# Kernel tuning notes

Measured on AMD Instinct MI355X. Metric: run time of the kernel, lower is better.

## Reference

```python
import jax, jax.numpy as jnp
import numpy as np

MAX_DISP = 4          # 9x9 displacement window -> 81 output channels
WIN = 2 * MAX_DISP + 1


def setup_inputs() -> dict:
    key = jax.random.key(0)
    k1, k2 = jax.random.split(key)
    B, C, H, W = 4, 256, 192, 192
    tensorFirst = jax.random.normal(k1, (B, C, H, W), dtype=jnp.float32)
    tensorSecond = jax.random.normal(k2, (B, C, H, W), dtype=jnp.float32)
    return {"tensorFirst": tensorFirst, "tensorSecond": tensorSecond}


def reference(tensorFirst, tensorSecond):
    # PWC-Net correlation: out[b, (dy+4)*9+(dx+4), y, x] =
    #   mean_c first[b,c,y,x] * second[b,c,y+dy,x+dx]  (second zero-padded by 4)
    B, C, H, W = tensorFirst.shape
    padded = jnp.pad(tensorSecond, ((0, 0), (0, 0), (MAX_DISP, MAX_DISP), (MAX_DISP, MAX_DISP)))
    outs = []
    for dy in range(WIN):
        for dx in range(WIN):
            shifted = padded[:, :, dy:dy + H, dx:dx + W]  # [B,C,H,W]
            outs.append(jnp.mean(tensorFirst * shifted, axis=1))  # [B,H,W]
    return jnp.stack(outs, axis=1)  # [B,81,H,W]
```

## Files before the change

### kernel.cpp

```cpp
#include <hip/hip_runtime.h>


#define MAXD 4
#define WINW 9
#define NDISP 81

constexpr int B_ = 4, C_ = 256, H_ = 192, W_ = 192;
constexpr int PHW = H_ * W_;
constexpr int YS = 3;
constexpr int DS = 3;
constexpr int XS = 64;
constexpr int VR = YS + DS - 1;
constexpr int NUT = 5;
constexpr int KB = 32;
constexpr int NK = C_ / KB;
constexpr int NTHREADS = 512;

constexpr int S_USHORT = VR * NUT * 512;
constexpr int F_USHORT = YS * 4 * 512;
constexpr int LDS_USHORT = S_USHORT + F_USHORT;
constexpr int S_TASKS = S_USHORT / 8;
constexpr int F_TASKS = F_USHORT / 8;

constexpr int NYS = H_ / YS;
constexpr int NDS = WINW / DS;
constexpr int NXS = W_ / XS;
constexpr int NBLK = B_ * NYS * NDS * NXS;
constexpr int PER_XCD = NBLK / 8;

typedef __attribute__((ext_vector_type(8))) short bf16x8;
typedef __attribute__((ext_vector_type(4))) float f32x4;

__device__ __forceinline__ unsigned f2bf(float f) {
    unsigned u = __float_as_uint(f);
    return (u + 0x7FFFu + ((u >> 16) & 1u)) >> 16;
}

__global__ __launch_bounds__(NTHREADS, 4)
void corr_kernel(const float* __restrict__ F, const float* __restrict__ S,
                 float* __restrict__ O) {
    __shared__ __align__(16) unsigned short lds[LDS_USHORT];

    const int tid  = threadIdx.x;
    const int lane = tid & 63;
    const int wid  = tid >> 6;
    const int xt   = wid & 3;
    const int uh   = wid >> 2;
    const int utw  = xt + uh;

    const int id = blockIdx.x;
    const int lg = (id & 7) * PER_XCD + (id >> 3);
    const int xs     = lg % NXS;
    const int t1     = lg / NXS;
    const int dstrip = t1 % NDS;
    const int t2     = t1 / NDS;
    const int ystrip = t2 % NYS;
    const int b      = t2 / NYS;
    const int Y0 = ystrip * YS, D0 = dstrip * DS, x0 = xs * XS;
    const int vbase = Y0 + D0 - MAXD;
    const int ubase = x0 - 8;

    const float* Fb = F + (long)b * C_ * PHW;
    const float* Sb = S + (long)b * C_ * PHW;

    const float* sP[4]; int sL[4]; bool sOk[4], sAct[4];
    #pragma unroll
    for (int q = 0; q < 4; ++q) {
        const int t   = tid + q * NTHREADS;
        const bool a  = (t < S_TASKS);
        const int tt  = a ? t : 0;
        const int u16 = tt & 15;
        const int kh  = (tt >> 4) & 3;
        const int rest = tt >> 6;
        const int ut  = rest % 5;
        const int vr  = rest / 5;
        const int v   = vbase + vr;
        const int u   = ubase + ut * 16 + u16;
        const bool inb = a && ((unsigned)v < (unsigned)H_) &&
                              ((unsigned)u < (unsigned)W_);
        sAct[q] = a;
        sOk[q]  = inb;
        sL[q]   = tt * 8;
        sP[q]   = Sb + (long)(kh * 8) * PHW + (long)(inb ? v : 0) * W_
                     + (inb ? u : 0);
    }
    const float* fP[2]; int fL[2]; bool fAct[2];
    #pragma unroll
    for (int q = 0; q < 2; ++q) {
        const int t   = tid + q * NTHREADS;
        const bool a  = (t < F_TASKS);
        const int tt  = a ? t : 0;
        const int x16 = tt & 15;
        const int kh  = (tt >> 4) & 3;
        const int rest = tt >> 6;
        const int xtq = rest & 3;
        const int yy  = rest >> 2;
        fAct[q] = a;
        fL[q]   = S_USHORT + tt * 8;
        fP[q]   = Fb + (long)(kh * 8) * PHW + (long)(Y0 + yy) * W_
                     + (x0 + xtq * 16 + x16);
    }

    f32x4 acc[3][3];
    #pragma unroll
    for (int yy = 0; yy < 3; ++yy)
        #pragma unroll
        for (int dd = 0; dd < 3; ++dd)
            acc[yy][dd] = (f32x4){0.f, 0.f, 0.f, 0.f};

    for (int step = 0; step < NK; ++step) {
        const int c0 = step * KB;
        #pragma unroll
        for (int q = 0; q < 4; ++q) {
            if (!sAct[q]) continue;
            unsigned w0 = 0, w1 = 0, w2 = 0, w3 = 0;
            if (sOk[q]) {
                const float* p = sP[q] + (long)c0 * PHW;
                float f[8];
                #pragma unroll
                for (int j = 0; j < 8; ++j) f[j] = p[j * PHW];
                w0 = f2bf(f[0]) | (f2bf(f[1]) << 16);
                w1 = f2bf(f[2]) | (f2bf(f[3]) << 16);
                w2 = f2bf(f[4]) | (f2bf(f[5]) << 16);
                w3 = f2bf(f[6]) | (f2bf(f[7]) << 16);
            }
            uint4 v; v.x = w0; v.y = w1; v.z = w2; v.w = w3;
            *(uint4*)(&lds[sL[q]]) = v;
        }
        #pragma unroll
        for (int q = 0; q < 2; ++q) {
            if (!fAct[q]) continue;
            const float* p = fP[q] + (long)c0 * PHW;
            float f[8];
            #pragma unroll
            for (int j = 0; j < 8; ++j) f[j] = p[j * PHW];
            uint4 v;
            v.x = f2bf(f[0]) | (f2bf(f[1]) << 16);
            v.y = f2bf(f[2]) | (f2bf(f[3]) << 16);
            v.z = f2bf(f[4]) | (f2bf(f[5]) << 16);
            v.w = f2bf(f[6]) | (f2bf(f[7]) << 16);
            *(uint4*)(&lds[fL[q]]) = v;
        }
        __syncthreads();

        bf16x8 A[5], Bf[3];
        #pragma unroll
        for (int vr = 0; vr < 5; ++vr)
            A[vr] = *(const bf16x8*)(&lds[(vr * 5 + utw) * 512 + lane * 8]);
        #pragma unroll
        for (int yy = 0; yy < 3; ++yy)
            Bf[yy] = *(const bf16x8*)(&lds[S_USHORT + (yy * 4 + xt) * 512
                                           + lane * 8]);
        #pragma unroll
        for (int yy = 0; yy < 3; ++yy)
            #pragma unroll
            for (int dd = 0; dd < 3; ++dd)
                acc[yy][dd] = __builtin_amdgcn_mfma_f32_16x16x32_bf16(
                    A[yy + dd], Bf[yy], acc[yy][dd], 0, 0, 0);

        if (step + 1 < NK) __syncthreads();
    }

    const float scale = 1.0f / (float)C_;
    const int col   = lane & 15;
    const int rowb  = (lane >> 4) * 4;
    const int x_abs = x0 + xt * 16 + col;
    #pragma unroll
    for (int r = 0; r < 4; ++r) {
        const int dx = uh * 16 + rowb + r - col - 4;
        if (0 <= dx && dx < WINW) {
            #pragma unroll
            for (int yy = 0; yy < 3; ++yy)
                #pragma unroll
                for (int dd = 0; dd < 3; ++dd) {
                    const int d = (D0 + dd) * WINW + dx;
                    O[((long)(b * NDISP + d) * H_ + (Y0 + yy)) * W_ + x_abs]
                        = acc[yy][dd][r] * scale;
                }
        }
    }
}

extern "C" void kernel_launch(void* const* d_in, const int* in_sizes, int n_in,
                              void* d_out, int out_size, void* d_ws, size_t ws_size,
                              hipStream_t stream) {
    const float* F = (const float*)d_in[0];
    const float* S = (const float*)d_in[1];
    float* O = (float*)d_out;
    dim3 grid(NBLK, 1, 1);
    dim3 block(NTHREADS);
    corr_kernel<<<grid, block, 0, stream>>>(F, S, O);
}
```

Measured before the change: 402.3 us.

## Prefetch next channel chunk of second tensor into registers and remap loads

The S-tile global loads for the next channel block are issued into registers before the barrier and compute of the current step, so their latency overlaps the MFMA work. The task-to-thread mapping is changed so consecutive lanes read consecutive x positions, which makes global loads coalesced. Out-of-bounds LDS slots are zeroed once instead of every step. The __syncthreads calls are replaced by a custom lgkmcnt-wait plus s_barrier. The cost is more register pressure from the sv buffer, which may hurt occupancy at the 4-waves launch bound.

```diff
diff --git a/kernel.cpp b/kernel.cpp
--- a/kernel.cpp
+++ b/kernel.cpp
@@ -19,8 +19,9 @@
 constexpr int S_USHORT = VR * NUT * 512;
 constexpr int F_USHORT = YS * 4 * 512;
 constexpr int LDS_USHORT = S_USHORT + F_USHORT;
-constexpr int S_TASKS = S_USHORT / 8;
-constexpr int F_TASKS = F_USHORT / 8;
+
+constexpr int S_TASKS = VR * 4 * 80;
+constexpr int F_TASKS = YS * 4 * 64;
 
 constexpr int NYS = H_ / YS;
 constexpr int NDS = WINW / DS;
@@ -34,6 +35,12 @@
 __device__ __forceinline__ unsigned f2bf(float f) {
     unsigned u = __float_as_uint(f);
     return (u + 0x7FFFu + ((u >> 16) & 1u)) >> 16;
+}
+
+__device__ __forceinline__ void wg_barrier_lds() {
+    asm volatile("s_waitcnt lgkmcnt(0)" ::: "memory");
+    __builtin_amdgcn_s_barrier();
+    asm volatile("" ::: "memory");
 }
 
 __global__ __launch_bounds__(NTHREADS, 4)
@@ -63,42 +70,43 @@
     const float* Fb = F + (long)b * C_ * PHW;
     const float* Sb = S + (long)b * C_ * PHW;
 
-    const float* sP[4]; int sL[4]; bool sOk[4], sAct[4];
+    unsigned sOff[4]; int sIdx[4]; bool sOk[4], sAct[4];
     #pragma unroll
     for (int q = 0; q < 4; ++q) {
         const int t   = tid + q * NTHREADS;
         const bool a  = (t < S_TASKS);
         const int tt  = a ? t : 0;
-        const int u16 = tt & 15;
-        const int kh  = (tt >> 4) & 3;
-        const int rest = tt >> 6;
-        const int ut  = rest % 5;
-        const int vr  = rest / 5;
+        const int u   = tt % 80;
+        const int rest = tt / 80;
+        const int kh  = rest & 3;
+        const int vr  = rest >> 2;
         const int v   = vbase + vr;
-        const int u   = ubase + ut * 16 + u16;
-        const bool inb = a && ((unsigned)v < (unsigned)H_) &&
-                              ((unsigned)u < (unsigned)W_);
-        sAct[q] = a;
-        sOk[q]  = inb;
-        sL[q]   = tt * 8;
-        sP[q]   = Sb + (long)(kh * 8) * PHW + (long)(inb ? v : 0) * W_
-                     + (inb ? u : 0);
-    }
-    const float* fP[2]; int fL[2]; bool fAct[2];
+        const int ua  = ubase + u;
+        const bool ok = a && ((unsigned)v < (unsigned)H_) &&
+                             ((unsigned)ua < (unsigned)W_);
+        sAct[q] = a; sOk[q] = ok;
+        sIdx[q] = (vr * 5 + (u >> 4)) * 512 + kh * 128 + (u & 15) * 8;
+        sOff[q] = (unsigned)(kh * 8 * PHW + (ok ? v : 0) * W_ + (ok ? ua : 0));
+    }
+    unsigned fOff[2]; int fIdx[2]; bool fAct[2];
     #pragma unroll
     for (int q = 0; q < 2; ++q) {
         const int t   = tid + q * NTHREADS;
         const bool a  = (t < F_TASKS);
         const int tt  = a ? t : 0;
-        const int x16 = tt & 15;
-        const int kh  = (tt >> 4) & 3;
-        const int rest = tt >> 6;
-        const int xtq = rest & 3;
-        const int yy  = rest >> 2;
+        const int x   = tt & 63;
+        const int kh  = (tt >> 6) & 3;
+        const int yy  = tt >> 8;
         fAct[q] = a;
-        fL[q]   = S_USHORT + tt * 8;
-        fP[q]   = Fb + (long)(kh * 8) * PHW + (long)(Y0 + yy) * W_
-                     + (x0 + xtq * 16 + x16);
+        fIdx[q] = S_USHORT + (yy * 4 + (x >> 4)) * 512 + kh * 128 + (x & 15) * 8;
+        fOff[q] = (unsigned)(kh * 8 * PHW + (Y0 + yy) * W_ + x0 + x);
+    }
+
+    {
+        uint4 z; z.x = z.y = z.z = z.w = 0u;
+        #pragma unroll
+        for (int q = 0; q < 4; ++q)
+            if (sAct[q] && !sOk[q]) *(uint4*)(&lds[sIdx[q]]) = z;
     }
 
     f32x4 acc[3][3];
@@ -108,40 +116,62 @@
         for (int dd = 0; dd < 3; ++dd)
             acc[yy][dd] = (f32x4){0.f, 0.f, 0.f, 0.f};
 
+    float sv[4][8];
+    #pragma unroll
+    for (int q = 0; q < 4; ++q) {
+        if (sOk[q]) {
+            const float* p = Sb + sOff[q];
+            #pragma unroll
+            for (int j = 0; j < 8; ++j) sv[q][j] = p[(long)j * PHW];
+        }
+        sOff[q] += KB * PHW;
+    }
+
     for (int step = 0; step < NK; ++step) {
-        const int c0 = step * KB;
+        float fv[2][8];
+        #pragma unroll
+        for (int q = 0; q < 2; ++q) {
+            if (fAct[q]) {
+                const float* p = Fb + fOff[q];
+                #pragma unroll
+                for (int j = 0; j < 8; ++j) fv[q][j] = p[(long)j * PHW];
+            }
+            fOff[q] += KB * PHW;
+        }
         #pragma unroll
         for (int q = 0; q < 4; ++q) {
-            if (!sAct[q]) continue;
-            unsigned w0 = 0, w1 = 0, w2 = 0, w3 = 0;
             if (sOk[q]) {
-                const float* p = sP[q] + (long)c0 * PHW;
-                float f[8];
-                #pragma unroll
-                for (int j = 0; j < 8; ++j) f[j] = p[j * PHW];
-                w0 = f2bf(f[0]) | (f2bf(f[1]) << 16);
-                w1 = f2bf(f[2]) | (f2bf(f[3]) << 16);
-                w2 = f2bf(f[4]) | (f2bf(f[5]) << 16);
-                w3 = f2bf(f[6]) | (f2bf(f[7]) << 16);
-            }
-            uint4 v; v.x = w0; v.y = w1; v.z = w2; v.w = w3;
-            *(uint4*)(&lds[sL[q]]) = v;
+                uint4 v;
+                v.x = f2bf(sv[q][0]) | (f2bf(sv[q][1]) << 16);
+                v.y = f2bf(sv[q][2]) | (f2bf(sv[q][3]) << 16);
+                v.z = f2bf(sv[q][4]) | (f2bf(sv[q][5]) << 16);
+                v.w = f2bf(sv[q][6]) | (f2bf(sv[q][7]) << 16);
+                *(uint4*)(&lds[sIdx[q]]) = v;
+            }
+        }
+        if (step + 1 < NK) {
+            #pragma unroll
+            for (int q = 0; q < 4; ++q) {
+                if (sOk[q]) {
+                    const float* p = Sb + sOff[q];
+                    #pragma unroll
+                    for (int j = 0; j < 8; ++j) sv[q][j] = p[(long)j * PHW];
+                }
+                sOff[q] += KB * PHW;
+            }
         }
         #pragma unroll
         for (int q = 0; q < 2; ++q) {
-            if (!fAct[q]) continue;
-            const float* p = fP[q] + (long)c0 * PHW;
-            float f[8];
-            #pragma unroll
-            for (int j = 0; j < 8; ++j) f[j] = p[j * PHW];
-            uint4 v;
-            v.x = f2bf(f[0]) | (f2bf(f[1]) << 16);
-            v.y = f2bf(f[2]) | (f2bf(f[3]) << 16);
-            v.z = f2bf(f[4]) | (f2bf(f[5]) << 16);
-            v.w = f2bf(f[6]) | (f2bf(f[7]) << 16);
-            *(uint4*)(&lds[fL[q]]) = v;
-        }
-        __syncthreads();
+            if (fAct[q]) {
+                uint4 v;
+                v.x = f2bf(fv[q][0]) | (f2bf(fv[q][1]) << 16);
+                v.y = f2bf(fv[q][2]) | (f2bf(fv[q][3]) << 16);
+                v.z = f2bf(fv[q][4]) | (f2bf(fv[q][5]) << 16);
+                v.w = f2bf(fv[q][6]) | (f2bf(fv[q][7]) << 16);
+                *(uint4*)(&lds[fIdx[q]]) = v;
+            }
+        }
+        wg_barrier_lds();
 
         bf16x8 A[5], Bf[3];
         #pragma unroll
@@ -158,7 +188,7 @@
                 acc[yy][dd] = __builtin_amdgcn_mfma_f32_16x16x32_bf16(
                     A[yy + dd], Bf[yy], acc[yy][dd], 0, 0, 0);
 
-        if (step + 1 < NK) __syncthreads();
+        wg_barrier_lds();
     }
 
     const float scale = 1.0f / (float)C_;
```

Measured after the change: 403.5 us. About the same (+0.3%).
